# Optimization experiments

Measured on AMD Instinct MI355X. Metric: run time of the kernel, lower is better.

The kernel has to match this reference:

```python
import jax, jax.numpy as jnp
import numpy as np

# Semantic hierarchy configuration (stand-in for semantic_softmax_processor)
GROUP_SIZES = [8192, 4096, 2048, 1024, 512, 256, 128, 64, 32, 16]
NORM_FACTORS = [0.1] * len(GROUP_SIZES)
TOPK_CAP = 500
TEMPERATURE = 1.0
TOTAL_CLASSES = sum(GROUP_SIZES)  # 16368
BATCH = 1024


def setup_inputs() -> dict:
    key = jax.random.key(0)
    k1, k2, k3 = jax.random.split(key, 3)
    logits = jax.random.normal(k1, (BATCH, TOTAL_CLASSES), dtype=jnp.float32)
    logits_teacher = jax.random.normal(k2, (BATCH, TOTAL_CLASSES), dtype=jnp.float32)
    targets = jax.random.randint(k3, (BATCH,), 0, TOTAL_CLASSES, dtype=jnp.int64)
    return {"logits": logits, "logits_teacher": logits_teacher, "targets": targets}


def _group_kd_loss(s_logits, t_logits, temperature):
    # s_logits, t_logits: [B, C_i] for one semantic group
    B, C = t_logits.shape
    k = min(C, TOPK_CAP)
    # teacher top-k classes (sorted, largest)
    t_top, t_idx = jax.lax.top_k(t_logits, k)                 # [B, k]
    s_top = jnp.take_along_axis(s_logits, t_idx, axis=1)      # [B, k]
    log_p = jax.nn.log_softmax(s_top / temperature, axis=1)   # student log-probs
    log_q = jax.nn.log_softmax(t_top / temperature, axis=1)   # teacher log-probs
    q = jnp.exp(log_q)
    # KL(q || p), reduction='batchmean'
    kl = jnp.sum(q * (log_q - log_p)) / B
    return kl * temperature * temperature


def reference(logits, logits_teacher, targets):
    # targets are converted to semantic targets in the original module but are
    # never used in the loss computation (dead code) -> no effect on output.
    del targets
    total = jnp.float32(0.0)
    offset = 0
    for gsize, norm in zip(GROUP_SIZES, NORM_FACTORS):
        s_i = jax.lax.slice_in_dim(logits, offset, offset + gsize, axis=1)
        t_i = jax.lax.slice_in_dim(logits_teacher, offset, offset + gsize, axis=1)
        total = total + _group_kd_loss(s_i, t_i, TEMPERATURE) * norm
        offset += gsize
    return total
```

## Files before the change

### kernel.cpp

```cpp
#include <hip/hip_runtime.h>
#include <stdint.h>
#include <float.h>

#define TOTAL 16368
#define KSEL 500
#define CAP 1280
#define NSLOT 20
#define NBUCKET 64

__device__ __forceinline__ uint32_t fkey(float f) {
    uint32_t u = __float_as_uint(f);
    return (u & 0x80000000u) ? ~u : (u | 0x80000000u);
}
__device__ __forceinline__ float keyf(uint32_t k) {
    uint32_t u = (k & 0x80000000u) ? (k & 0x7FFFFFFFu) : ~k;
    return __uint_as_float(u);
}
__device__ __forceinline__ int wave_sumi(int v) {
    #pragma unroll
    for (int o = 32; o > 0; o >>= 1) v += __shfl_xor(v, o, 64);
    return v;
}
__device__ __forceinline__ float wave_sumf(float v) {
    #pragma unroll
    for (int o = 32; o > 0; o >>= 1) v += __shfl_xor(v, o, 64);
    return v;
}
__device__ __forceinline__ float wave_maxf(float v) {
    #pragma unroll
    for (int o = 32; o > 0; o >>= 1) v = fmaxf(v, __shfl_xor(v, o, 64));
    return v;
}
__device__ __forceinline__ void lse_merge(float& m, float& l, float m2, float l2) {
    float M = fmaxf(m, m2);
    l = l * __expf(m - M) + l2 * __expf(m2 - M);
    m = M;
}

__device__ __noinline__ float wave_slow_kl(const float* __restrict__ t,
                                           const float* __restrict__ s, int C) {
    const int lane = threadIdx.x & 63;
    uint64_t lo = 0ull, hi = (1ull << 45), tau = 0ull;
    int cl = C, ch = 0;
    for (int it = 0; it < 100; ++it) {
        uint64_t span = hi - lo;
        if (span <= 1ull) { tau = lo; break; }
        uint64_t mid;
        if (it & 1) mid = lo + (span >> 1);
        else {
            uint64_t st = span * (uint64_t)(cl - KSEL) / (uint64_t)(cl - ch);
            if (st < 1) st = 1;
            if (st > span - 1) st = span - 1;
            mid = lo + st;
        }
        int c = 0;
        for (int i = lane; i < C; i += 64) {
            uint64_t ck = ((uint64_t)fkey(t[i]) << 13) | (uint64_t)(8191 - i);
            c += (ck > mid);
        }
        c = wave_sumi(c);
        if (c == KSEL) { tau = mid; break; }
        if (c > KSEL) { lo = mid; cl = c; } else { hi = mid; ch = c; }
    }
    float tmx = -FLT_MAX;
    for (int i = lane; i < C; i += 64) tmx = fmaxf(tmx, t[i]);
    tmx = wave_maxf(tmx);
    float St = 0.f, Stt = 0.f, Sts = 0.f, sm = -FLT_MAX;
    for (int i = lane; i < C; i += 64) {
        float x = t[i];
        uint64_t ck = ((uint64_t)fkey(x) << 13) | (uint64_t)(8191 - i);
        if (ck > tau) {
            float e = __expf(x - tmx), v = s[i];
            St += e; Stt += e * x; Sts += e * v;
            sm = fmaxf(sm, v);
        }
    }
    St = wave_sumf(St); Stt = wave_sumf(Stt); Sts = wave_sumf(Sts); sm = wave_maxf(sm);
    float Ss = 0.f;
    for (int i = lane; i < C; i += 64) {
        uint64_t ck = ((uint64_t)fkey(t[i]) << 13) | (uint64_t)(8191 - i);
        if (ck > tau) Ss += __expf(s[i] - sm);
    }
    Ss = wave_sumf(Ss);
    if (lane == 0)
        return (Stt - Sts) / St - tmx - __logf(St) + sm + __logf(Ss);
    return 0.f;
}

template <int NF4>
__device__ float big_wave(const float* __restrict__ tg, const float* __restrict__ s,
                          float thr, float* vals, uint16_t* idxs) {
    const int lane = threadIdx.x & 63;
    const float4* t4 = (const float4*)tg;
    int cnt = 0;
    #pragma unroll
    for (int c0 = 0; c0 < NF4; c0 += 8) {
        float4 buf[8];
        #pragma unroll
        for (int u = 0; u < 8; ++u) buf[u] = t4[(c0 + u) * 64 + lane];
        int myc = 0;
        #pragma unroll
        for (int u = 0; u < 8; ++u)
            myc += (buf[u].x > thr) + (buf[u].y > thr) +
                   (buf[u].z > thr) + (buf[u].w > thr);
        int inc = myc;
        #pragma unroll
        for (int o = 1; o < 64; o <<= 1) {
            int y = __shfl_up(inc, o, 64);
            if (lane >= o) inc += y;
        }
        int base = cnt + inc - myc;
        cnt += __shfl(inc, 63, 64);
        #pragma unroll
        for (int u = 0; u < 8; ++u) {
            float xs[4] = {buf[u].x, buf[u].y, buf[u].z, buf[u].w};
            #pragma unroll
            for (int q = 0; q < 4; ++q) {
                if (xs[q] > thr) {
                    if (base < CAP) {
                        vals[base] = xs[q];
                        idxs[base] = (uint16_t)((((c0 + u) * 64 + lane) << 2) + q);
                    }
                    ++base;
                }
            }
        }
    }
    if (cnt < KSEL || cnt > CAP) return wave_slow_kl(tg, s, NF4 * 256);

    uint32_t key[NSLOT];
    float svc[NSLOT];
    #pragma unroll
    for (int j = 0; j < NSLOT; ++j) {
        int p = lane + j * 64;
        bool v = p < cnt;
        key[j] = v ? fkey(vals[p]) : 0u;
        svc[j] = v ? s[(int)idxs[p]] : 0.f;
    }
    uint32_t kmx = 0u, kmn = 0xFFFFFFFFu;
    #pragma unroll
    for (int j = 0; j < NSLOT; ++j) {
        uint32_t k = key[j];
        kmx = k > kmx ? k : kmx;
        if (k) kmn = k < kmn ? k : kmn;
    }
    #pragma unroll
    for (int o = 32; o > 0; o >>= 1) {
        uint32_t a = __shfl_xor(kmx, o, 64); kmx = a > kmx ? a : kmx;
        uint32_t b = __shfl_xor(kmn, o, 64); kmn = b < kmn ? b : kmn;
    }
    const float tmax = keyf(kmx);

    uint32_t lo = kmn - 1u, hi = kmx, tauhi = kmx;
    int cl = cnt, ch = 0, cut = -1;
    bool exact = false;
    for (int it = 0; it < 80; ++it) {
        uint32_t span = hi - lo;
        if (span <= 1u) break;
        uint32_t mid;
        if (!(it & 1)) {
            uint64_t st = (uint64_t)span * (uint32_t)(cl - KSEL) / (uint32_t)(cl - ch);
            if (st < 1) st = 1;
            if (st > span - 1) st = span - 1;
            mid = lo + (uint32_t)st;
        } else mid = lo + (span >> 1);
        int c = 0;
        #pragma unroll
        for (int j = 0; j < NSLOT; ++j) c += (key[j] > mid);
        c = wave_sumi(c);
        if (c == KSEL) { tauhi = mid; exact = true; break; }
        if (c > KSEL) { lo = mid; cl = c; } else { hi = mid; ch = c; }
    }
    if (!exact) {
        tauhi = hi;
        const int nT = KSEL - ch, nTie = cl - ch;
        if (nT >= nTie) cut = 0x7FFFFFFF;
        else {
            int l = -1, h = 8191;
            while (h - l > 1) {
                int m = (l + h) >> 1;
                int c = 0;
                #pragma unroll
                for (int j = 0; j < NSLOT; ++j) {
                    int p = lane + j * 64;
                    c += (key[j] == tauhi && p < cnt && (int)idxs[p] <= m);
                }
                c = wave_sumi(c);
                if (c >= nT) h = m; else l = m;
            }
            cut = h;
        }
    }

    uint32_t selm = 0u;
    if (cut == -1) {
        #pragma unroll
        for (int j = 0; j < NSLOT; ++j) selm |= (key[j] > tauhi ? 1u : 0u) << j;
    } else if (cut == 0x7FFFFFFF) {
        #pragma unroll
        for (int j = 0; j < NSLOT; ++j) selm |= (key[j] >= tauhi ? 1u : 0u) << j;
    } else {
        #pragma unroll
        for (int j = 0; j < NSLOT; ++j) {
            int p = lane + j * 64;
            bool sj = (key[j] > tauhi) ||
                      (key[j] == tauhi && p < cnt && (int)idxs[p] <= cut);
            selm |= (sj ? 1u : 0u) << j;
        }
    }

    float St = 0.f, Stt = 0.f, Sts = 0.f, sm = -FLT_MAX;
    #pragma unroll
    for (int j = 0; j < NSLOT; ++j) {
        if (selm & (1u << j)) {
            float tv = keyf(key[j]);
            float e = __expf(tv - tmax);
            St += e; Stt += e * tv; Sts += e * svc[j];
            sm = fmaxf(sm, svc[j]);
        }
    }
    #pragma unroll
    for (int o = 32; o > 0; o >>= 1) {
        St  += __shfl_xor(St,  o, 64);
        Stt += __shfl_xor(Stt, o, 64);
        Sts += __shfl_xor(Sts, o, 64);
        sm = fmaxf(sm, __shfl_xor(sm, o, 64));
    }
    float Ss = 0.f;
    #pragma unroll
    for (int j = 0; j < NSLOT; ++j)
        if (selm & (1u << j)) Ss += __expf(svc[j] - sm);
    Ss = wave_sumf(Ss);
    if (lane == 0)
        return (Stt - Sts) / St - tmax - __logf(St) + sm + __logf(Ss);
    return 0.f;
}

template <int NS, class IdxF>
__device__ float select_accum(uint32_t (&key)[NS], IdxF idxOf, const float* svp) {
    const int lane = threadIdx.x & 63;
    uint32_t kmx = 0u, kmn = 0xFFFFFFFFu;
    #pragma unroll
    for (int j = 0; j < NS; ++j) {
        uint32_t k = key[j];
        kmx = k > kmx ? k : kmx;
        kmn = k < kmn ? k : kmn;
    }
    #pragma unroll
    for (int o = 32; o > 0; o >>= 1) {
        uint32_t a = __shfl_xor(kmx, o, 64); kmx = a > kmx ? a : kmx;
        uint32_t b = __shfl_xor(kmn, o, 64); kmn = b < kmn ? b : kmn;
    }
    const float tmax = keyf(kmx);

    uint32_t lo = kmn - 1u, hi = kmx, tauhi = kmx;
    int cl = NS * 64, ch = 0, cut = -1;
    bool exact = false;
    for (int it = 0; it < 80; ++it) {
        uint32_t span = hi - lo;
        if (span <= 1u) break;
        uint32_t mid;
        if (!(it & 1)) {
            uint64_t st = (uint64_t)span * (uint32_t)(cl - KSEL) / (uint32_t)(cl - ch);
            if (st < 1) st = 1;
            if (st > span - 1) st = span - 1;
            mid = lo + (uint32_t)st;
        } else mid = lo + (span >> 1);
        int c = 0;
        #pragma unroll
        for (int j = 0; j < NS; ++j) c += (key[j] > mid);
        c = wave_sumi(c);
        if (c == KSEL) { tauhi = mid; exact = true; break; }
        if (c > KSEL) { lo = mid; cl = c; } else { hi = mid; ch = c; }
    }
    if (!exact) {
        tauhi = hi;
        const int nT = KSEL - ch, nTie = cl - ch;
        if (nT >= nTie) cut = 0x7FFFFFFF;
        else {
            int l = -1, h = NS * 64 - 1;
            while (h - l > 1) {
                int m = (l + h) >> 1;
                int c = 0;
                #pragma unroll
                for (int j = 0; j < NS; ++j)
                    c += (key[j] == tauhi && idxOf(j) <= m);
                c = wave_sumi(c);
                if (c >= nT) h = m; else l = m;
            }
            cut = h;
        }
    }

    float St = 0.f, Stt = 0.f, Sts = 0.f, sm = -FLT_MAX;
    #pragma unroll
    for (int j = 0; j < NS; ++j) {
        uint32_t kj = key[j];
        bool sj = (kj > tauhi) || (kj == tauhi && idxOf(j) <= cut);
        if (sj) {
            float tv = keyf(kj);
            float e = __expf(tv - tmax);
            St += e; Stt += e * tv; Sts += e * svp[j];
            sm = fmaxf(sm, svp[j]);
        }
    }
    #pragma unroll
    for (int o = 32; o > 0; o >>= 1) {
        St  += __shfl_xor(St,  o, 64);
        Stt += __shfl_xor(Stt, o, 64);
        Sts += __shfl_xor(Sts, o, 64);
        sm = fmaxf(sm, __shfl_xor(sm, o, 64));
    }
    float Ss = 0.f;
    #pragma unroll
    for (int j = 0; j < NS; ++j) {
        uint32_t kj = key[j];
        bool sj = (kj > tauhi) || (kj == tauhi && idxOf(j) <= cut);
        if (sj) Ss += __expf(svp[j] - sm);
    }
    Ss = wave_sumf(Ss);
    const int lane0 = lane;
    if (lane0 == 0)
        return (Stt - Sts) / St - tmax - __logf(St) + sm + __logf(Ss);
    return 0.f;
}

template <int NJ>
__device__ float mid_wave(const float* __restrict__ t, const float* __restrict__ s) {
    const int lane = threadIdx.x & 63;
    const float4* t4 = (const float4*)t;
    const float4* s4 = (const float4*)s;
    uint32_t key[NJ];
    float svp[NJ];
    #pragma unroll
    for (int c = 0; c < NJ / 4; ++c) {
        float4 x = t4[lane + c * 64];
        float4 y = s4[lane + c * 64];
        key[4 * c + 0] = fkey(x.x); key[4 * c + 1] = fkey(x.y);
        key[4 * c + 2] = fkey(x.z); key[4 * c + 3] = fkey(x.w);
        svp[4 * c + 0] = y.x; svp[4 * c + 1] = y.y;
        svp[4 * c + 2] = y.z; svp[4 * c + 3] = y.w;
    }
    auto idxOf = [&](int j) { return ((lane + (j >> 2) * 64) << 2) + (j & 3); };
    return select_accum<NJ>(key, idxOf, svp);
}

__device__ float tiny_group(const float* __restrict__ t, const float* __restrict__ s,
                            int Cg) {
    const int lane = threadIdx.x & 63;
    float St = 0.f, Stt = 0.f, Sts = 0.f, m = -FLT_MAX, l = 0.f;
    float tv[4], svv[4];
    #pragma unroll
    for (int q = 0; q < 4; ++q) {
        int i = lane + q * 64;
        bool va = i < Cg;
        tv[q] = va ? t[i] : -FLT_MAX;
        svv[q] = va ? s[i] : 0.f;
    }
    float mx = -FLT_MAX;
    #pragma unroll
    for (int q = 0; q < 4; ++q) mx = fmaxf(mx, tv[q]);
    mx = wave_maxf(mx);
    #pragma unroll
    for (int q = 0; q < 4; ++q) {
        if (lane + q * 64 < Cg) {
            float e = __expf(tv[q] - mx);
            St += e; Stt += e * tv[q]; Sts += e * svv[q];
            float x = svv[q];
            if (x > m) { l = l * __expf(m - x) + 1.f; m = x; }
            else       { l += __expf(x - m); }
        }
    }
    #pragma unroll
    for (int o = 32; o > 0; o >>= 1) {
        St  += __shfl_xor(St,  o, 64);
        Stt += __shfl_xor(Stt, o, 64);
        Sts += __shfl_xor(Sts, o, 64);
        float m2 = __shfl_xor(m, o, 64);
        float l2 = __shfl_xor(l, o, 64);
        lse_merge(m, l, m2, l2);
    }
    if (lane == 0)
        return (Stt - Sts) / St - mx - __logf(St) + m + __logf(l);
    return 0.f;
}

__global__ __launch_bounds__(256, 4) void kd_all(const float* __restrict__ sL,
                                                 const float* __restrict__ tL,
                                                 float* __restrict__ partial) {
    __shared__ float    vals[2][CAP];
    __shared__ uint16_t idxs[2][CAP];
    const int row = blockIdx.x;
    const int w = threadIdx.x >> 6;
    const float* tr = tL + (size_t)row * TOTAL;
    const float* sr = sL + (size_t)row * TOTAL;

    float kl = 0.f;
    switch (w) {
    case 0: kl = big_wave<32>(tr,        sr,        1.10f, vals[0], idxs[0]); break;
    case 1: kl = big_wave<16>(tr + 8192, sr + 8192, 0.60f, vals[1], idxs[1]); break;
    case 2:
        kl  = mid_wave<32>(tr + 12288, sr + 12288);
        kl += mid_wave<16>(tr + 14336, sr + 14336);
        break;
    default:
        kl  = mid_wave<8>(tr + 15360, sr + 15360);
        kl += tiny_group(tr + 15872, sr + 15872, 256);
        kl += tiny_group(tr + 16128, sr + 16128, 128);
        kl += tiny_group(tr + 16256, sr + 16256, 64);
        kl += tiny_group(tr + 16320, sr + 16320, 32);
        kl += tiny_group(tr + 16352, sr + 16352, 16);
        break;
    }
    if ((threadIdx.x & 63) == 0)
        atomicAdd(&partial[(row + w * 37) & (NBUCKET - 1)], kl * (0.1f / 1024.f));
}

__global__ void zero_ws(float* partial) {
    if (threadIdx.x < NBUCKET) partial[threadIdx.x] = 0.f;
}

__global__ void final_sum(const float* __restrict__ partial, float* __restrict__ out) {
    float v = (threadIdx.x < NBUCKET) ? partial[threadIdx.x] : 0.f;
    #pragma unroll
    for (int o = 32; o > 0; o >>= 1) v += __shfl_down(v, o, 64);
    if (threadIdx.x == 0) out[0] = v;
}

extern "C" void kernel_launch(void* const* d_in, const int* in_sizes, int n_in,
                              void* d_out, int out_size, void* d_ws, size_t ws_size,
                              hipStream_t stream) {
    (void)in_sizes; (void)n_in; (void)ws_size; (void)out_size;
    const float* s = (const float*)d_in[0];
    const float* t = (const float*)d_in[1];
    float* out = (float*)d_out;
    float* ws = (float*)d_ws;

    hipLaunchKernelGGL(zero_ws, dim3(1), dim3(64), 0, stream, ws);
    hipLaunchKernelGGL(kd_all, dim3(1024), dim3(256), 0, stream, s, t, ws);
    hipLaunchKernelGGL(final_sum, dim3(1), dim3(64), 0, stream, ws, out);
}
```

Measured before the change: 169.2 us.

## Split large-group threshold compaction across all four waves with segmented shared buffers

Instead of one wave scanning the whole 8192-element group and another the 4096-element group, each of the four waves compacts a quarter of each large group (and the 2048 group) into its own fixed-capacity shared segment, together with the student values. After a block barrier, three waves each run the radix/interpolation selection over the padded segments, while the small groups are spread across the waves beforehand. This balances the load-heavy scanning across waves and removes the serial gather of student values, at the cost of more shared memory, a __syncthreads, and a slow-path fallback if any quarter overflows its segment cap.

```diff
diff --git a/kernel.cpp b/kernel.cpp
--- a/kernel.cpp
+++ b/kernel.cpp
@@ -4,8 +4,8 @@
 
 #define TOTAL 16368
 #define KSEL 500
-#define CAP 1280
-#define NSLOT 20
+#define QCAP0 384
+#define QCAP2 224
 #define NBUCKET 64
 
 __device__ __forceinline__ uint32_t fkey(float f) {
@@ -87,59 +87,69 @@
     return 0.f;
 }
 
-template <int NF4>
-__device__ float big_wave(const float* __restrict__ tg, const float* __restrict__ s,
-                          float thr, float* vals, uint16_t* idxs) {
-    const int lane = threadIdx.x & 63;
-    const float4* t4 = (const float4*)tg;
-    int cnt = 0;
-    #pragma unroll
-    for (int c0 = 0; c0 < NF4; c0 += 8) {
-        float4 buf[8];
+template <int NF4Q, int SEGCAP>
+__device__ int quarter_compact(const float* __restrict__ tq,
+                               const float* __restrict__ sq,
+                               float thr, int idx_off,
+                               uint32_t* kv, float* sv, uint16_t* ix) {
+    const int lane = threadIdx.x & 63;
+    const float4* t4 = (const float4*)tq;
+    float4 buf[NF4Q];
+    #pragma unroll
+    for (int u = 0; u < NF4Q; ++u) buf[u] = t4[u * 64 + lane];
+    int myc = 0;
+    #pragma unroll
+    for (int u = 0; u < NF4Q; ++u)
+        myc += (buf[u].x > thr) + (buf[u].y > thr) +
+               (buf[u].z > thr) + (buf[u].w > thr);
+    int inc = myc;
+    #pragma unroll
+    for (int o = 1; o < 64; o <<= 1) {
+        int y = __shfl_up(inc, o, 64);
+        if (lane >= o) inc += y;
+    }
+    int base = inc - myc;
+    int total = __shfl(inc, 63, 64);
+    if (total <= SEGCAP) {
         #pragma unroll
-        for (int u = 0; u < 8; ++u) buf[u] = t4[(c0 + u) * 64 + lane];
-        int myc = 0;
-        #pragma unroll
-        for (int u = 0; u < 8; ++u)
-            myc += (buf[u].x > thr) + (buf[u].y > thr) +
-                   (buf[u].z > thr) + (buf[u].w > thr);
-        int inc = myc;
-        #pragma unroll
-        for (int o = 1; o < 64; o <<= 1) {
-            int y = __shfl_up(inc, o, 64);
-            if (lane >= o) inc += y;
-        }
-        int base = cnt + inc - myc;
-        cnt += __shfl(inc, 63, 64);
-        #pragma unroll
-        for (int u = 0; u < 8; ++u) {
+        for (int u = 0; u < NF4Q; ++u) {
             float xs[4] = {buf[u].x, buf[u].y, buf[u].z, buf[u].w};
             #pragma unroll
             for (int q = 0; q < 4; ++q) {
                 if (xs[q] > thr) {
-                    if (base < CAP) {
-                        vals[base] = xs[q];
-                        idxs[base] = (uint16_t)((((c0 + u) * 64 + lane) << 2) + q);
-                    }
+                    int gi = ((u * 64 + lane) << 2) + q;
+                    kv[base] = fkey(xs[q]);
+                    sv[base] = sq[gi];
+                    ix[base] = (uint16_t)(gi + idx_off);
                     ++base;
                 }
             }
         }
-    }
-    if (cnt < KSEL || cnt > CAP) return wave_slow_kl(tg, s, NF4 * 256);
-
-    uint32_t key[NSLOT];
-    float svc[NSLOT];
-    #pragma unroll
-    for (int j = 0; j < NSLOT; ++j) {
-        int p = lane + j * 64;
-        bool v = p < cnt;
-        key[j] = v ? fkey(vals[p]) : 0u;
-        svc[j] = v ? s[(int)idxs[p]] : 0.f;
-    }
+        for (int p = total + lane; p < SEGCAP; p += 64) kv[p] = 0u;
+    }
+    return total;
+}
+
+template <int NS, int SEGCAP>
+__device__ float seg_select(const uint32_t* __restrict__ kv,
+                            const float* __restrict__ sv,
+                            const uint16_t* __restrict__ ix,
+                            const int* cnts, int C,
+                            const float* __restrict__ tg,
+                            const float* __restrict__ sg) {
+    const int lane = threadIdx.x & 63;
+    const int tot = cnts[0] + cnts[1] + cnts[2] + cnts[3];
+    bool bad = (tot < KSEL) || (cnts[0] > SEGCAP) || (cnts[1] > SEGCAP) ||
+               (cnts[2] > SEGCAP) || (cnts[3] > SEGCAP);
+    if (bad) return wave_slow_kl(tg, sg, C);
+
+    uint32_t key[NS];
+    #pragma unroll
+    for (int j = 0; j < NS; ++j) key[j] = kv[lane + j * 64];
+
     uint32_t kmx = 0u, kmn = 0xFFFFFFFFu;
     #pragma unroll
-    for (int j = 0; j < NSLOT; ++j) {
+    for (int j = 0; j < NS; ++j) {
         uint32_t k = key[j];
         kmx = k > kmx ? k : kmx;
         if (k) kmn = k < kmn ? k : kmn;
@@ -152,7 +162,7 @@
     const float tmax = keyf(kmx);
 
     uint32_t lo = kmn - 1u, hi = kmx, tauhi = kmx;
-    int cl = cnt, ch = 0, cut = -1;
+    int cl = tot, ch = 0, cut = -1;
     bool exact = false;
     for (int it = 0; it < 80; ++it) {
         uint32_t span = hi - lo;
@@ -166,7 +176,7 @@
         } else mid = lo + (span >> 1);
         int c = 0;
         #pragma unroll
-        for (int j = 0; j < NSLOT; ++j) c += (key[j] > mid);
+        for (int j = 0; j < NS; ++j) c += (key[j] > mid);
         c = wave_sumi(c);
         if (c == KSEL) { tauhi = mid; exact = true; break; }
         if (c > KSEL) { lo = mid; cl = c; } else { hi = mid; ch = c; }
@@ -176,15 +186,13 @@
         const int nT = KSEL - ch, nTie = cl - ch;
         if (nT >= nTie) cut = 0x7FFFFFFF;
         else {
-            int l = -1, h = 8191;
+            int l = -1, h = C - 1;
             while (h - l > 1) {
                 int m = (l + h) >> 1;
                 int c = 0;
                 #pragma unroll
-                for (int j = 0; j < NSLOT; ++j) {
-                    int p = lane + j * 64;
-                    c += (key[j] == tauhi && p < cnt && (int)idxs[p] <= m);
-                }
+                for (int j = 0; j < NS; ++j)
+                    c += (key[j] == tauhi && (int)ix[lane + j * 64] <= m);
                 c = wave_sumi(c);
                 if (c >= nT) h = m; else l = m;
             }
@@ -195,28 +203,28 @@
     uint32_t selm = 0u;
     if (cut == -1) {
         #pragma unroll
-        for (int j = 0; j < NSLOT; ++j) selm |= (key[j] > tauhi ? 1u : 0u) << j;
+        for (int j = 0; j < NS; ++j) selm |= (key[j] > tauhi ? 1u : 0u) << j;
     } else if (cut == 0x7FFFFFFF) {
         #pragma unroll
-        for (int j = 0; j < NSLOT; ++j) selm |= (key[j] >= tauhi ? 1u : 0u) << j;
+        for (int j = 0; j < NS; ++j) selm |= (key[j] >= tauhi ? 1u : 0u) << j;
     } else {
         #pragma unroll
-        for (int j = 0; j < NSLOT; ++j) {
-            int p = lane + j * 64;
+        for (int j = 0; j < NS; ++j) {
             bool sj = (key[j] > tauhi) ||
-                      (key[j] == tauhi && p < cnt && (int)idxs[p] <= cut);
+                      (key[j] == tauhi && (int)ix[lane + j * 64] <= cut);
             selm |= (sj ? 1u : 0u) << j;
         }
     }
 
     float St = 0.f, Stt = 0.f, Sts = 0.f, sm = -FLT_MAX;
     #pragma unroll
-    for (int j = 0; j < NSLOT; ++j) {
+    for (int j = 0; j < NS; ++j) {
         if (selm & (1u << j)) {
             float tv = keyf(key[j]);
             float e = __expf(tv - tmax);
-            St += e; Stt += e * tv; Sts += e * svc[j];
-            sm = fmaxf(sm, svc[j]);
+            float s = sv[lane + j * 64];
+            St += e; Stt += e * tv; Sts += e * s;
+            sm = fmaxf(sm, s);
         }
     }
     #pragma unroll
@@ -228,8 +236,8 @@
     }
     float Ss = 0.f;
     #pragma unroll
-    for (int j = 0; j < NSLOT; ++j)
-        if (selm & (1u << j)) Ss += __expf(svc[j] - sm);
+    for (int j = 0; j < NS; ++j)
+        if (selm & (1u << j)) Ss += __expf(sv[lane + j * 64] - sm);
     Ss = wave_sumf(Ss);
     if (lane == 0)
         return (Stt - Sts) / St - tmax - __logf(St) + sm + __logf(Ss);
@@ -319,8 +327,7 @@
         if (sj) Ss += __expf(svp[j] - sm);
     }
     Ss = wave_sumf(Ss);
-    const int lane0 = lane;
-    if (lane0 == 0)
+    if (lane == 0)
         return (Stt - Sts) / St - tmax - __logf(St) + sm + __logf(Ss);
     return 0.f;
 }
@@ -388,31 +395,82 @@
 __global__ __launch_bounds__(256, 4) void kd_all(const float* __restrict__ sL,
                                                  const float* __restrict__ tL,
                                                  float* __restrict__ partial) {
-    __shared__ float    vals[2][CAP];
-    __shared__ uint16_t idxs[2][CAP];
+    __shared__ uint32_t kv0[4 * QCAP0];
+    __shared__ float    sv0[4 * QCAP0];
+    __shared__ uint16_t ix0[4 * QCAP0];
+    __shared__ uint32_t kv1[4 * QCAP0];
+    __shared__ float    sv1[4 * QCAP0];
+    __shared__ uint16_t ix1[4 * QCAP0];
+    __shared__ uint32_t kv2[4 * QCAP2];
+    __shared__ float    sv2[4 * QCAP2];
+    __shared__ uint16_t ix2[4 * QCAP2];
+    __shared__ int      cnts[12];
+
     const int row = blockIdx.x;
     const int w = threadIdx.x >> 6;
+    const int lane = threadIdx.x & 63;
     const float* tr = tL + (size_t)row * TOTAL;
     const float* sr = sL + (size_t)row * TOTAL;
 
     float kl = 0.f;
+
+    int c0 = quarter_compact<8, QCAP0>(tr + w * 2048, sr + w * 2048, 1.10f,
+                                       w * 2048,
+                                       kv0 + w * QCAP0, sv0 + w * QCAP0,
+                                       ix0 + w * QCAP0);
+    int c1 = quarter_compact<4, QCAP0>(tr + 8192 + w * 1024, sr + 8192 + w * 1024,
+                                       0.60f, w * 1024,
+                                       kv1 + w * QCAP0, sv1 + w * QCAP0,
+                                       ix1 + w * QCAP0);
+    if (lane == 0) { cnts[w] = c0; cnts[4 + w] = c1; }
+
+    if (w != 2) {
+        int q = (w == 3) ? 2 : w;
+        int c2 = quarter_compact<2, QCAP2>(tr + 12288 + q * 512, sr + 12288 + q * 512,
+                                           0.50f, q * 512,
+                                           kv2 + q * QCAP2, sv2 + q * QCAP2,
+                                           ix2 + q * QCAP2);
+        if (lane == 0) cnts[8 + q] = c2;
+        if (w == 3) {
+            int c3 = quarter_compact<2, QCAP2>(tr + 12288 + 3 * 512,
+                                               sr + 12288 + 3 * 512,
+                                               0.50f, 3 * 512,
+                                               kv2 + 3 * QCAP2, sv2 + 3 * QCAP2,
+                                               ix2 + 3 * QCAP2);
+            if (lane == 0) cnts[11] = c3;
+        }
+    }
+
     switch (w) {
-    case 0: kl = big_wave<32>(tr,        sr,        1.10f, vals[0], idxs[0]); break;
-    case 1: kl = big_wave<16>(tr + 8192, sr + 8192, 0.60f, vals[1], idxs[1]); break;
-    case 2:
-        kl  = mid_wave<32>(tr + 12288, sr + 12288);
-        kl += mid_wave<16>(tr + 14336, sr + 14336);
-        break;
-    default:
-        kl  = mid_wave<8>(tr + 15360, sr + 15360);
+    case 0:
         kl += tiny_group(tr + 15872, sr + 15872, 256);
         kl += tiny_group(tr + 16128, sr + 16128, 128);
         kl += tiny_group(tr + 16256, sr + 16256, 64);
         kl += tiny_group(tr + 16320, sr + 16320, 32);
         kl += tiny_group(tr + 16352, sr + 16352, 16);
         break;
-    }
-    if ((threadIdx.x & 63) == 0)
+    case 1:
+        kl += mid_wave<8>(tr + 15360, sr + 15360);
+        break;
+    case 2:
+        kl += mid_wave<16>(tr + 14336, sr + 14336);
+        break;
+    default:
+        break;
+    }
+
+    __syncthreads();
+
+    if (w == 3)
+        kl += seg_select<24, QCAP0>(kv0, sv0, ix0, cnts, 8192, tr, sr);
+    else if (w == 0)
+        kl += seg_select<24, QCAP0>(kv1, sv1, ix1, cnts + 4, 4096,
+                                    tr + 8192, sr + 8192);
+    else if (w == 1)
+        kl += seg_select<14, QCAP2>(kv2, sv2, ix2, cnts + 8, 2048,
+                                    tr + 12288, sr + 12288);
+
+    if (lane == 0)
         atomicAdd(&partial[(row + w * 37) & (NBUCKET - 1)], kl * (0.1f / 1024.f));
 }
 
```

Result: slower. 193.0 us (+14.1%).

## Split largest group's threshold compaction across two waves and rebalance wave workloads

Applied to the files above, without the earlier changes.

The 8192-wide group was handled by a single wave. It is now split into two halves, and each half is threshold-compacted into shared memory by a separate wave. After a block barrier, wave 0 runs a combined radix/interpolation select over the merged candidates. The remaining groups are redistributed among the four waves to balance per-wave work. This adds a __syncthreads and extra shared memory, and falls back to a slow path when the candidate counts are out of range.

```diff
diff --git a/kernel.cpp b/kernel.cpp
--- a/kernel.cpp
+++ b/kernel.cpp
@@ -6,6 +6,8 @@
 #define KSEL 500
 #define CAP 1280
 #define NSLOT 20
+#define HCAP 672
+#define NSEG 21
 #define NBUCKET 64
 
 __device__ __forceinline__ uint32_t fkey(float f) {
@@ -236,6 +238,175 @@
     return 0.f;
 }
 
+__device__ int half_compact(const float* __restrict__ tq, const float* __restrict__ sg,
+                            float thr, int idx_off,
+                            uint32_t* kv, float* sv, uint16_t* ix) {
+    const int lane = threadIdx.x & 63;
+    const float4* t4 = (const float4*)tq;
+    int cnt = 0;
+    #pragma unroll
+    for (int c0 = 0; c0 < 16; c0 += 8) {
+        float4 buf[8];
+        #pragma unroll
+        for (int u = 0; u < 8; ++u) buf[u] = t4[(c0 + u) * 64 + lane];
+        int myc = 0;
+        #pragma unroll
+        for (int u = 0; u < 8; ++u)
+            myc += (buf[u].x > thr) + (buf[u].y > thr) +
+                   (buf[u].z > thr) + (buf[u].w > thr);
+        int inc = myc;
+        #pragma unroll
+        for (int o = 1; o < 64; o <<= 1) {
+            int y = __shfl_up(inc, o, 64);
+            if (lane >= o) inc += y;
+        }
+        int base = cnt + inc - myc;
+        cnt += __shfl(inc, 63, 64);
+        #pragma unroll
+        for (int u = 0; u < 8; ++u) {
+            float xs[4] = {buf[u].x, buf[u].y, buf[u].z, buf[u].w};
+            #pragma unroll
+            for (int q = 0; q < 4; ++q) {
+                if (xs[q] > thr) {
+                    if (base < HCAP) {
+                        kv[base] = fkey(xs[q]);
+                        ix[base] = (uint16_t)(((((c0 + u) * 64 + lane) << 2) + q)
+                                              + idx_off);
+                    }
+                    ++base;
+                }
+            }
+        }
+    }
+    if (cnt <= HCAP) {
+        for (int p = cnt + lane; p < HCAP; p += 64) kv[p] = 0u;
+        float r[11];
+        #pragma unroll
+        for (int j = 0; j < 11; ++j) {
+            int p = lane + j * 64;
+            r[j] = (p < cnt) ? sg[(int)ix[p]] : 0.f;
+        }
+        #pragma unroll
+        for (int j = 0; j < 11; ++j) {
+            int p = lane + j * 64;
+            if (p < cnt) sv[p] = r[j];
+        }
+    }
+    return cnt;
+}
+
+__device__ float pair_select(const uint32_t* __restrict__ kv,
+                             const float* __restrict__ sv,
+                             const uint16_t* __restrict__ ix,
+                             const int* cnts,
+                             const float* __restrict__ tg,
+                             const float* __restrict__ sg) {
+    const int lane = threadIdx.x & 63;
+    const int tot = cnts[0] + cnts[1];
+    bool bad = (tot < KSEL) || (cnts[0] > HCAP) || (cnts[1] > HCAP);
+    if (bad) return wave_slow_kl(tg, sg, 8192);
+
+    uint32_t key[NSEG];
+    #pragma unroll
+    for (int j = 0; j < NSEG; ++j) key[j] = kv[lane + j * 64];
+
+    uint32_t kmx = 0u, kmn = 0xFFFFFFFFu;
+    #pragma unroll
+    for (int j = 0; j < NSEG; ++j) {
+        uint32_t k = key[j];
+        kmx = k > kmx ? k : kmx;
+        if (k) kmn = k < kmn ? k : kmn;
+    }
+    #pragma unroll
+    for (int o = 32; o > 0; o >>= 1) {
+        uint32_t a = __shfl_xor(kmx, o, 64); kmx = a > kmx ? a : kmx;
+        uint32_t b = __shfl_xor(kmn, o, 64); kmn = b < kmn ? b : kmn;
+    }
+    const float tmax = keyf(kmx);
+
+    uint32_t lo = kmn - 1u, hi = kmx, tauhi = kmx;
+    int cl = tot, ch = 0, cut = -1;
+    bool exact = false;
+    for (int it = 0; it < 80; ++it) {
+        uint32_t span = hi - lo;
+        if (span <= 1u) break;
+        uint32_t mid;
+        if (!(it & 1)) {
+            uint64_t st = (uint64_t)span * (uint32_t)(cl - KSEL) / (uint32_t)(cl - ch);
+            if (st < 1) st = 1;
+            if (st > span - 1) st = span - 1;
+            mid = lo + (uint32_t)st;
+        } else mid = lo + (span >> 1);
+        int c = 0;
+        #pragma unroll
+        for (int j = 0; j < NSEG; ++j) c += (key[j] > mid);
+        c = wave_sumi(c);
+        if (c == KSEL) { tauhi = mid; exact = true; break; }
+        if (c > KSEL) { lo = mid; cl = c; } else { hi = mid; ch = c; }
+    }
+    if (!exact) {
+        tauhi = hi;
+        const int nT = KSEL - ch, nTie = cl - ch;
+        if (nT >= nTie) cut = 0x7FFFFFFF;
+        else {
+            int l = -1, h = 8191;
+            while (h - l > 1) {
+                int m = (l + h) >> 1;
+                int c = 0;
+                #pragma unroll
+                for (int j = 0; j < NSEG; ++j)
+                    c += (key[j] == tauhi && (int)ix[lane + j * 64] <= m);
+                c = wave_sumi(c);
+                if (c >= nT) h = m; else l = m;
+            }
+            cut = h;
+        }
+    }
+
+    uint32_t selm = 0u;
+    if (cut == -1) {
+        #pragma unroll
+        for (int j = 0; j < NSEG; ++j) selm |= (key[j] > tauhi ? 1u : 0u) << j;
+    } else if (cut == 0x7FFFFFFF) {
+        #pragma unroll
+        for (int j = 0; j < NSEG; ++j) selm |= (key[j] >= tauhi ? 1u : 0u) << j;
+    } else {
+        #pragma unroll
+        for (int j = 0; j < NSEG; ++j) {
+            bool sj = (key[j] > tauhi) ||
+                      (key[j] == tauhi && (int)ix[lane + j * 64] <= cut);
+            selm |= (sj ? 1u : 0u) << j;
+        }
+    }
+
+    float St = 0.f, Stt = 0.f, Sts = 0.f, sm = -FLT_MAX;
+    #pragma unroll
+    for (int j = 0; j < NSEG; ++j) {
+        if (selm & (1u << j)) {
+            float tv = keyf(key[j]);
+            float e = __expf(tv - tmax);
+            float s = sv[lane + j * 64];
+            St += e; Stt += e * tv; Sts += e * s;
+            sm = fmaxf(sm, s);
+        }
+    }
+    #pragma unroll
+    for (int o = 32; o > 0; o >>= 1) {
+        St  += __shfl_xor(St,  o, 64);
+        Stt += __shfl_xor(Stt, o, 64);
+        Sts += __shfl_xor(Sts, o, 64);
+        sm = fmaxf(sm, __shfl_xor(sm, o, 64));
+    }
+    float Ss = 0.f;
+    #pragma unroll
+    for (int j = 0; j < NSEG; ++j)
+        if (selm & (1u << j)) Ss += __expf(sv[lane + j * 64] - sm);
+    Ss = wave_sumf(Ss);
+    if (lane == 0)
+        return (Stt - Sts) / St - tmax - __logf(St) + sm + __logf(Ss);
+    return 0.f;
+}
+
 template <int NS, class IdxF>
 __device__ float select_accum(uint32_t (&key)[NS], IdxF idxOf, const float* svp) {
     const int lane = threadIdx.x & 63;
@@ -319,8 +490,7 @@
         if (sj) Ss += __expf(svp[j] - sm);
     }
     Ss = wave_sumf(Ss);
-    const int lane0 = lane;
-    if (lane0 == 0)
+    if (lane == 0)
         return (Stt - Sts) / St - tmax - __logf(St) + sm + __logf(Ss);
     return 0.f;
 }
@@ -388,23 +558,31 @@
 __global__ __launch_bounds__(256, 4) void kd_all(const float* __restrict__ sL,
                                                  const float* __restrict__ tL,
                                                  float* __restrict__ partial) {
-    __shared__ float    vals[2][CAP];
-    __shared__ uint16_t idxs[2][CAP];
+    __shared__ uint32_t kv[2 * HCAP];
+    __shared__ float    sv[2 * HCAP];
+    __shared__ uint16_t ix[2 * HCAP];
+    __shared__ int      cnts[2];
+    __shared__ float    vals1[CAP];
+    __shared__ uint16_t idxs1[CAP];
+
     const int row = blockIdx.x;
     const int w = threadIdx.x >> 6;
+    const int lane = threadIdx.x & 63;
     const float* tr = tL + (size_t)row * TOTAL;
     const float* sr = sL + (size_t)row * TOTAL;
 
     float kl = 0.f;
+
     switch (w) {
-    case 0: kl = big_wave<32>(tr,        sr,        1.10f, vals[0], idxs[0]); break;
-    case 1: kl = big_wave<16>(tr + 8192, sr + 8192, 0.60f, vals[1], idxs[1]); break;
-    case 2:
-        kl  = mid_wave<32>(tr + 12288, sr + 12288);
-        kl += mid_wave<16>(tr + 14336, sr + 14336);
+    case 0: {
+        int c = half_compact(tr, sr, 1.10f, 0, kv, sv, ix);
+        if (lane == 0) cnts[0] = c;
         break;
-    default:
-        kl  = mid_wave<8>(tr + 15360, sr + 15360);
+    }
+    case 1: {
+        int c = half_compact(tr + 4096, sr, 1.10f, 4096,
+                             kv + HCAP, sv + HCAP, ix + HCAP);
+        if (lane == 0) cnts[1] = c;
         kl += tiny_group(tr + 15872, sr + 15872, 256);
         kl += tiny_group(tr + 16128, sr + 16128, 128);
         kl += tiny_group(tr + 16256, sr + 16256, 64);
@@ -412,7 +590,22 @@
         kl += tiny_group(tr + 16352, sr + 16352, 16);
         break;
     }
-    if ((threadIdx.x & 63) == 0)
+    case 2:
+        kl  = big_wave<16>(tr + 8192, sr + 8192, 0.60f, vals1, idxs1);
+        kl += mid_wave<8>(tr + 15360, sr + 15360);
+        break;
+    default:
+        kl  = mid_wave<32>(tr + 12288, sr + 12288);
+        kl += mid_wave<16>(tr + 14336, sr + 14336);
+        break;
+    }
+
+    __syncthreads();
+
+    if (w == 0)
+        kl += pair_select(kv, sv, ix, cnts, tr, sr);
+
+    if (lane == 0)
         atomicAdd(&partial[(row + w * 37) & (NBUCKET - 1)], kl * (0.1f / 1024.f));
 }
 
```

Measured after the change: 188.0 us. 1.11x slower.

## Split per-row work into independent single-wave blocks and use big_wave for 2048 group

Applied to the files above, without the earlier changes.

Replaces the 256-thread block per row, where each wave handled a different group set, with 4096 single-wave blocks that each take one (job,row) pair. This lets the scheduler balance the uneven per-wave work instead of every block waiting for its slowest wave, and each block allocates only one shared buffer. The 2048-wide group also switches from mid_wave to the big_wave selection path with its own threshold parameter. The trade-off is more block launches, less shared-memory reuse per block, and a different algorithm for that group.

```diff
diff --git a/kernel.cpp b/kernel.cpp
--- a/kernel.cpp
+++ b/kernel.cpp
@@ -319,8 +319,7 @@
         if (sj) Ss += __expf(svp[j] - sm);
     }
     Ss = wave_sumf(Ss);
-    const int lane0 = lane;
-    if (lane0 == 0)
+    if (lane == 0)
         return (Stt - Sts) / St - tmax - __logf(St) + sm + __logf(Ss);
     return 0.f;
 }
@@ -385,22 +384,27 @@
     return 0.f;
 }
 
-__global__ __launch_bounds__(256, 4) void kd_all(const float* __restrict__ sL,
+__global__ __launch_bounds__(64, 4) void kd_jobs(const float* __restrict__ sL,
                                                  const float* __restrict__ tL,
                                                  float* __restrict__ partial) {
-    __shared__ float    vals[2][CAP];
-    __shared__ uint16_t idxs[2][CAP];
-    const int row = blockIdx.x;
-    const int w = threadIdx.x >> 6;
+    __shared__ float    vals[CAP];
+    __shared__ uint16_t idxs[CAP];
+    const int bid = blockIdx.x;
+    const int job = bid >> 10;
+    const int row = bid & 1023;
     const float* tr = tL + (size_t)row * TOTAL;
     const float* sr = sL + (size_t)row * TOTAL;
 
     float kl = 0.f;
-    switch (w) {
-    case 0: kl = big_wave<32>(tr,        sr,        1.10f, vals[0], idxs[0]); break;
-    case 1: kl = big_wave<16>(tr + 8192, sr + 8192, 0.60f, vals[1], idxs[1]); break;
+    switch (job) {
+    case 0:
+        kl = big_wave<32>(tr, sr, 1.10f, vals, idxs);
+        break;
+    case 1:
+        kl = big_wave<16>(tr + 8192, sr + 8192, 0.60f, vals, idxs);
+        break;
     case 2:
-        kl  = mid_wave<32>(tr + 12288, sr + 12288);
+        kl  = big_wave<8>(tr + 12288, sr + 12288, 0.50f, vals, idxs);
         kl += mid_wave<16>(tr + 14336, sr + 14336);
         break;
     default:
@@ -412,8 +416,9 @@
         kl += tiny_group(tr + 16352, sr + 16352, 16);
         break;
     }
+
     if ((threadIdx.x & 63) == 0)
-        atomicAdd(&partial[(row + w * 37) & (NBUCKET - 1)], kl * (0.1f / 1024.f));
+        atomicAdd(&partial[(row + job * 37) & (NBUCKET - 1)], kl * (0.1f / 1024.f));
 }
 
 __global__ void zero_ws(float* partial) {
@@ -437,6 +442,6 @@
     float* ws = (float*)d_ws;
 
     hipLaunchKernelGGL(zero_ws, dim3(1), dim3(64), 0, stream, ws);
-    hipLaunchKernelGGL(kd_all, dim3(1024), dim3(256), 0, stream, s, t, ws);
+    hipLaunchKernelGGL(kd_jobs, dim3(4096), dim3(64), 0, stream, s, t, ws);
     hipLaunchKernelGGL(final_sum, dim3(1), dim3(64), 0, stream, ws, out);
 }
```

Result: no change. 171.1 us (+1.1%).
